# Kernel optimization log

Measured on AMD Instinct MI355X. Metric: run time of the kernel, lower is better.

## Reference

```python
import jax, jax.numpy as jnp
import numpy as np

B, S, D = 4, 2048, 1024
H, HD = 8, 128
EPS = 1e-5
NEG = -1e30


def layernorm(x, w, b):
    mu = jnp.mean(x, axis=-1, keepdims=True)
    var = jnp.mean(jnp.square(x - mu), axis=-1, keepdims=True)
    return (x - mu) * jax.lax.rsqrt(var + EPS) * w + b


def rmsnorm(x, w):
    ms = jnp.mean(jnp.square(x), axis=-1, keepdims=True)
    return x * jax.lax.rsqrt(ms + EPS) * w


def setup_inputs() -> dict:
    key = jax.random.key(0)
    ks = jax.random.split(key, 8)
    scale = 0.02
    return {
        "layer_input": jax.random.normal(ks[0], (B, S, D), jnp.float32),
        "positions": jnp.broadcast_to(jnp.arange(S, dtype=jnp.int32), (B, S)),
        "ln_in_w": jnp.ones((D,), jnp.float32),
        "ln_in_b": jnp.zeros((D,), jnp.float32),
        "W_uvqk": jax.random.normal(ks[1], (D, 4 * H * HD), jnp.float32) * scale,
        "b_uvqk": jax.random.normal(ks[2], (4 * H * HD,), jnp.float32) * scale,
        "ln_out_w": jnp.ones((H * HD,), jnp.float32),
        "ln_out_b": jnp.zeros((H * HD,), jnp.float32),
        "W_proj": jax.random.normal(ks[3], (H * HD, D), jnp.float32) * scale,
        "rms_w": jnp.ones((D,), jnp.float32),
        "W1": jax.random.normal(ks[4], (D, 2 * D), jnp.float32) * scale,
        "W2": jax.random.normal(ks[5], (D, D), jnp.float32) * scale,
    }


def reference(layer_input, positions, ln_in_w, ln_in_b, W_uvqk, b_uvqk,
              ln_out_w, ln_out_b, W_proj, rms_w, W1, W2):
    # --- HSTU attention block ---
    normed = layernorm(layer_input, ln_in_w, ln_in_b)              # [B,S,D]
    mixed = jax.nn.silu(normed @ W_uvqk + b_uvqk)                  # [B,S,4*H*HD]
    user, value, query, key = jnp.split(mixed, 4, axis=-1)
    q = query.reshape(B, S, H, HD)
    k = key.reshape(B, S, H, HD)
    v = value.reshape(B, S, H, HD)
    alpha = 1.0 / np.sqrt(HD).astype(np.float32)
    scores = jnp.einsum("bqhd,bkhd->bhqk", q, k) * alpha           # [B,H,S,S]
    causal = jnp.tril(jnp.ones((S, S), bool))
    scores = jnp.where(causal, scores, NEG)
    probs = jax.nn.softmax(scores, axis=-1)
    attn = jnp.einsum("bhqk,bkhd->bqhd", probs, v).reshape(B, S, H * HD)
    # output norm * user gate, then projection
    parallel = user * layernorm(attn, ln_out_w, ln_out_b)          # [B,S,H*HD]
    layer_output = parallel @ W_proj                               # [B,S,D]
    # --- residual add + RMSNorm + SwiGLU FFN ---
    summed = layer_output + layer_input
    ffn_in = rmsnorm(summed, rms_w)
    h = ffn_in @ W1                                                # [B,S,2D]
    a, b = jnp.split(h, 2, axis=-1)                                # a <- w3, b <- w1
    ffn_out = (jax.nn.silu(a) * b) @ W2
    return ffn_out + layer_output
```

## Files before the change

kernel.cpp:

```cpp
#include <hip/hip_runtime.h>
#include <stdint.h>

typedef unsigned short u16;
typedef __bf16 bf16x8_t __attribute__((ext_vector_type(8)));
typedef float f32x4_t __attribute__((ext_vector_type(4)));

#define D_MODEL 1024
#define SEQ 2048
#define BATCH 4
#define NROWS (BATCH * SEQ)
#define HDIM 128

constexpr int EPI_UVQK = 0;
constexpr int EPI_F32 = 1;
constexpr int EPI_BF16 = 2;
constexpr int EPI_ADD_F32 = 3;

__device__ __forceinline__ float bf2f(u16 u) {
  union { unsigned int i; float f; } v; v.i = ((unsigned int)u) << 16; return v.f;
}
__device__ __forceinline__ u16 f2bf(float f) {
  union { float f; unsigned int i; } v; v.f = f;
  unsigned int r = (v.i + 0x7FFFu + ((v.i >> 16) & 1u)) >> 16;
  return (u16)r;
}
__device__ __forceinline__ float silu_f(float x) { return x / (1.0f + __expf(-x)); }

__device__ __forceinline__ void load_lds16(const void* g, void* l) {
  auto gp = (const __attribute__((address_space(1))) char*)(uintptr_t)g;
  auto lp = (__attribute__((address_space(3))) char*)(uint32_t)(uintptr_t)l;
  __builtin_amdgcn_global_load_lds(gp, lp, 16, 0, 0);
}

__device__ __forceinline__ void block_sum2(float& a, float& b, float* sm) {
  #pragma unroll
  for (int off = 32; off > 0; off >>= 1) {
    a += __shfl_xor(a, off, 64);
    b += __shfl_xor(b, off, 64);
  }
  const int w = threadIdx.x >> 6;
  if ((threadIdx.x & 63) == 0) { sm[w] = a; sm[4 + w] = b; }
  __syncthreads();
  a = sm[0] + sm[1] + sm[2] + sm[3];
  b = sm[4] + sm[5] + sm[6] + sm[7];
}

__global__ __launch_bounds__(256)
void k_wconv(const float* __restrict__ W, u16* __restrict__ Wt, int K, int N) {
  __shared__ float tile[32][33];
  const int n0 = blockIdx.x * 32, k0 = blockIdx.y * 32;
  const int tx = threadIdx.x & 31, ty = threadIdx.x >> 5;
  #pragma unroll
  for (int i = 0; i < 4; i++)
    tile[ty + 8 * i][tx] = W[(size_t)(k0 + ty + 8 * i) * N + n0 + tx];
  __syncthreads();
  #pragma unroll
  for (int i = 0; i < 4; i++)
    Wt[(size_t)(n0 + ty + 8 * i) * K + k0 + tx] = f2bf(tile[tx][ty + 8 * i]);
}

__global__ __launch_bounds__(256)
void k_ln_in(const float* __restrict__ X, const float* __restrict__ w,
             const float* __restrict__ b, u16* __restrict__ Y) {
  __shared__ float sm[8];
  const int row = blockIdx.x, t = threadIdx.x;
  const float4 v = ((const float4*)(X + (size_t)row * D_MODEL))[t];
  float s = v.x + v.y + v.z + v.w;
  float ss = v.x * v.x + v.y * v.y + v.z * v.z + v.w * v.w;
  block_sum2(s, ss, sm);
  const float mu = s * (1.0f / D_MODEL);
  const float var = ss * (1.0f / D_MODEL) - mu * mu;
  const float rs = rsqrtf(var + 1e-5f);
  const float4 wv = ((const float4*)w)[t];
  const float4 bv = ((const float4*)b)[t];
  ushort4 o;
  o.x = f2bf((v.x - mu) * rs * wv.x + bv.x);
  o.y = f2bf((v.y - mu) * rs * wv.y + bv.y);
  o.z = f2bf((v.z - mu) * rs * wv.z + bv.z);
  o.w = f2bf((v.w - mu) * rs * wv.w + bv.w);
  ((ushort4*)(Y + (size_t)row * D_MODEL))[t] = o;
}

__global__ __launch_bounds__(256)
void k_gated(const u16* __restrict__ attn, const u16* __restrict__ mixed,
             const float* __restrict__ w, const float* __restrict__ b,
             u16* __restrict__ out) {
  __shared__ float sm[8];
  const int row = blockIdx.x, t = threadIdx.x;
  const ushort4 av = ((const ushort4*)(attn + (size_t)row * D_MODEL))[t];
  const float x0 = bf2f(av.x), x1 = bf2f(av.y), x2 = bf2f(av.z), x3 = bf2f(av.w);
  float s = x0 + x1 + x2 + x3;
  float ss = x0 * x0 + x1 * x1 + x2 * x2 + x3 * x3;
  block_sum2(s, ss, sm);
  const float mu = s * (1.0f / D_MODEL);
  const float rs = rsqrtf(ss * (1.0f / D_MODEL) - mu * mu + 1e-5f);
  const ushort4 uv = ((const ushort4*)(mixed + (size_t)row * 4096))[t];
  const float4 wv = ((const float4*)w)[t];
  const float4 bv = ((const float4*)b)[t];
  ushort4 o;
  o.x = f2bf(bf2f(uv.x) * ((x0 - mu) * rs * wv.x + bv.x));
  o.y = f2bf(bf2f(uv.y) * ((x1 - mu) * rs * wv.y + bv.y));
  o.z = f2bf(bf2f(uv.z) * ((x2 - mu) * rs * wv.z + bv.z));
  o.w = f2bf(bf2f(uv.w) * ((x3 - mu) * rs * wv.w + bv.w));
  ((ushort4*)(out + (size_t)row * D_MODEL))[t] = o;
}

__global__ __launch_bounds__(256)
void k_rms(const float* __restrict__ lo, const float* __restrict__ li,
           const float* __restrict__ w, u16* __restrict__ out) {
  __shared__ float sm[8];
  const int row = blockIdx.x, t = threadIdx.x;
  const float4 a = ((const float4*)(lo + (size_t)row * D_MODEL))[t];
  const float4 bq = ((const float4*)(li + (size_t)row * D_MODEL))[t];
  const float x0 = a.x + bq.x, x1 = a.y + bq.y, x2 = a.z + bq.z, x3 = a.w + bq.w;
  float ss = x0 * x0 + x1 * x1 + x2 * x2 + x3 * x3, dummy = 0.f;
  block_sum2(ss, dummy, sm);
  const float rs = rsqrtf(ss * (1.0f / D_MODEL) + 1e-5f);
  const float4 wv = ((const float4*)w)[t];
  ushort4 o;
  o.x = f2bf(x0 * rs * wv.x);
  o.y = f2bf(x1 * rs * wv.y);
  o.z = f2bf(x2 * rs * wv.z);
  o.w = f2bf(x3 * rs * wv.w);
  ((ushort4*)(out + (size_t)row * D_MODEL))[t] = o;
}

__global__ __launch_bounds__(256)
void k_silumul(const u16* __restrict__ h, u16* __restrict__ g) {
  const int row = blockIdx.x, t = threadIdx.x;
  const ushort4 a = ((const ushort4*)(h + (size_t)row * 2048))[t];
  const ushort4 b = ((const ushort4*)(h + (size_t)row * 2048 + 1024))[t];
  ushort4 o;
  o.x = f2bf(silu_f(bf2f(a.x)) * bf2f(b.x));
  o.y = f2bf(silu_f(bf2f(a.y)) * bf2f(b.y));
  o.z = f2bf(silu_f(bf2f(a.z)) * bf2f(b.z));
  o.w = f2bf(silu_f(bf2f(a.w)) * bf2f(b.w));
  ((ushort4*)(g + (size_t)row * D_MODEL))[t] = o;
}

template <int EPI>
__global__ __launch_bounds__(256, 2)
void k_gemm(const u16* __restrict__ A, const u16* __restrict__ Bt,
            void* __restrict__ Cout, const float* __restrict__ bias,
            const float* __restrict__ addsrc,
            u16* __restrict__ kc, u16* __restrict__ vtc,
            int M, int N, int K) {
  __shared__ u16 As[128 * 64];
  __shared__ u16 Bs[128 * 64];
  const int t = threadIdx.x, lane = t & 63, w = t >> 6;
  const int l15 = lane & 15, l4 = lane >> 4;
  const int wr = w >> 1, wc = w & 1;
  const int m0 = blockIdx.x * 128, n0 = blockIdx.y * 128;
  const int lr = lane >> 3, lc = lane & 7;
  const int swz = (lc ^ lr) * 8;

  f32x4_t acc[4][4];
  #pragma unroll
  for (int mi = 0; mi < 4; mi++)
    #pragma unroll
    for (int ni = 0; ni < 4; ni++) {
      acc[mi][ni][0] = 0.f; acc[mi][ni][1] = 0.f; acc[mi][ni][2] = 0.f; acc[mi][ni][3] = 0.f;
    }

  const u16* Ab = A + (size_t)m0 * K + swz;
  const u16* Bb = Bt + (size_t)n0 * K + swz;

  for (int kt = 0; kt < K; kt += 64) {
    #pragma unroll
    for (int j = 0; j < 4; j++) {
      const size_t rr = (size_t)((w * 4 + j) * 8 + lr);
      load_lds16(Ab + rr * K + kt, &As[(w * 4 + j) * 512]);
      load_lds16(Bb + rr * K + kt, &Bs[(w * 4 + j) * 512]);
    }
    __syncthreads();
    #pragma unroll
    for (int kk = 0; kk < 2; kk++) {
      bf16x8_t af[4], bf[4];
      #pragma unroll
      for (int mi = 0; mi < 4; mi++) {
        const int row = wr * 64 + mi * 16 + l15;
        const int cph = (kk * 4 + l4) ^ (row & 7);
        af[mi] = *(const bf16x8_t*)&As[row * 64 + cph * 8];
      }
      #pragma unroll
      for (int ni = 0; ni < 4; ni++) {
        const int row = wc * 64 + ni * 16 + l15;
        const int cph = (kk * 4 + l4) ^ (row & 7);
        bf[ni] = *(const bf16x8_t*)&Bs[row * 64 + cph * 8];
      }
      #pragma unroll
      for (int mi = 0; mi < 4; mi++)
        #pragma unroll
        for (int ni = 0; ni < 4; ni++)
          acc[mi][ni] = __builtin_amdgcn_mfma_f32_16x16x32_bf16(af[mi], bf[ni], acc[mi][ni], 0, 0, 0);
    }
    __syncthreads();
  }

  #pragma unroll
  for (int mi = 0; mi < 4; mi++) {
    #pragma unroll
    for (int ni = 0; ni < 4; ni++) {
      const int col = n0 + wc * 64 + ni * 16 + l15;
      float bv = 0.f;
      if constexpr (EPI == EPI_UVQK) bv = bias[col];
      if constexpr (EPI == EPI_UVQK) {
        const int rowb = m0 + wr * 64 + mi * 16 + l4 * 4;
        u16 c4[4];
        #pragma unroll
        for (int r = 0; r < 4; r++) c4[r] = f2bf(silu_f(acc[mi][ni][r] + bv));
        if (col < 1024 || (col >= 2048 && col < 3072)) {
          #pragma unroll
          for (int r = 0; r < 4; r++)
            ((u16*)Cout)[(size_t)(rowb + r) * N + col] = c4[r];
        } else if (col < 2048) {
          const int h = (col - 1024) >> 7, d = (col - 1024) & 127;
          const int bI = rowb >> 11, seqr = rowb & 2047;
          const size_t off = ((size_t)(bI * 8 + h) * 32 + (seqr >> 6)) * 8192 + d * 64 + (seqr & 63);
          *(ushort4*)&vtc[off] = *(const ushort4*)c4;
        } else {
          const int h = (col - 3072) >> 7, d = (col - 3072) & 127;
          const int bI = rowb >> 11, seqr = rowb & 2047;
          #pragma unroll
          for (int r = 0; r < 4; r++)
            kc[((size_t)(bI * 8 + h) * 2048 + seqr + r) * 128 + d] = c4[r];
        }
      } else {
        #pragma unroll
        for (int r = 0; r < 4; r++) {
          const size_t row = (size_t)(m0 + wr * 64 + mi * 16 + l4 * 4 + r);
          float v = acc[mi][ni][r];
          if constexpr (EPI == EPI_BF16) {
            ((u16*)Cout)[row * N + col] = f2bf(v);
          } else if constexpr (EPI == EPI_F32) {
            ((float*)Cout)[row * N + col] = v;
          } else {
            ((float*)Cout)[row * N + col] = v + addsrc[row * N + col];
          }
        }
      }
    }
  }
}

__global__ __launch_bounds__(256, 2)
void k_attn(const u16* __restrict__ mixed, const u16* __restrict__ Kc,
            const u16* __restrict__ Vtc, u16* __restrict__ attnb,
            u16* __restrict__ o_part, float* __restrict__ ml) {
  __shared__ u16 Ks[64 * 128];
  __shared__ u16 Vts[128 * 64];
  __shared__ u16 Ps[4 * 16 * 64];
  const int t = threadIdx.x, lane = t & 63, w = t >> 6;
  const int l15 = lane & 15, l4 = lane >> 4;
  const int f = blockIdx.x;
  const int v = (f & 7) * 96 + (f >> 3);
  const int ci = v % 24, bh = v / 24;
  const int bI = bh >> 3, h = bh & 7;
  int qt, ch;
  if (ci < 16) { qt = 15 - (ci >> 1); ch = ci & 1; }
  else { qt = 23 - ci; ch = 0; }
  const bool split = (qt >= 8);
  const int qb = qt * 128;
  const int nt_all = 2 * qt + 2;
  const int t0 = (split && ch == 1) ? (qt + 1) : 0;
  const int t1 = (split && ch == 0) ? (qt + 1) : nt_all;

  const u16* base = mixed + (size_t)bI * SEQ * 4096;
  const int qcol = 2 * D_MODEL + h * HDIM;
  const int qrow0 = qb + w * 32;
  const u16* Kh = Kc + (size_t)bh * SEQ * 128;
  const u16* Vh = Vtc + (size_t)bh * 32 * 8192;

  const int nk = lane;

  bf16x8_t qf[2][4];
  #pragma unroll
  for (int mi = 0; mi < 2; mi++) {
    const u16* qp = base + (size_t)(qrow0 + mi * 16 + l15) * 4096 + qcol + l4 * 8;
    #pragma unroll
    for (int ks = 0; ks < 4; ks++) qf[mi][ks] = *(const bf16x8_t*)(qp + ks * 32);
  }

  f32x4_t o[2][8];
  #pragma unroll
  for (int mi = 0; mi < 2; mi++)
    #pragma unroll
    for (int df = 0; df < 8; df++) { o[mi][df][0] = 0.f; o[mi][df][1] = 0.f; o[mi][df][2] = 0.f; o[mi][df][3] = 0.f; }
  float mrun[2][4], lrun[2][4];
  #pragma unroll
  for (int mi = 0; mi < 2; mi++)
    #pragma unroll
    for (int r = 0; r < 4; r++) { mrun[mi][r] = -1e30f; lrun[mi][r] = 0.f; }

  const float alpha = 0.08838834764831845f;

  auto stage = [&](int tile) {
    const u16* Kt = Kh + (size_t)(tile * 64) * 128;
    const u16* Vt = Vh + (size_t)tile * 8192;
    #pragma unroll
    for (int j = 0; j < 4; j++) {
      const int slot = j * 4 + w;
      const int kr = slot * 4 + (nk >> 4), gk = nk & 15;
      load_lds16(Kt + kr * 128 + ((gk ^ (kr & 7)) * 8), &Ks[slot * 512]);
      const int d = slot * 8 + (nk >> 3), gv = nk & 7;
      load_lds16(Vt + d * 64 + ((gv ^ (d & 7) ^ ((d >> 3) & 7)) * 8), &Vts[slot * 512]);
    }
  };

  for (int it = t0; it < t1; it++) {
    const int kb = it * 64;
    stage(it);
    __syncthreads();

    const bool active = (kb <= qrow0 + 31);
    const bool needmask = (kb + 63 > qrow0);
    if (active) {
      f32x4_t s[2][4];
      #pragma unroll
      for (int mi = 0; mi < 2; mi++)
        #pragma unroll
        for (int ni = 0; ni < 4; ni++) { s[mi][ni][0] = 0.f; s[mi][ni][1] = 0.f; s[mi][ni][2] = 0.f; s[mi][ni][3] = 0.f; }
      #pragma unroll
      for (int ks = 0; ks < 4; ks++) {
        bf16x8_t kf[4];
        #pragma unroll
        for (int ni = 0; ni < 4; ni++) {
          const int key = ni * 16 + l15;
          const int cph = (ks * 4 + l4) ^ (key & 7);
          kf[ni] = *(const bf16x8_t*)&Ks[key * 128 + cph * 8];
        }
        #pragma unroll
        for (int mi = 0; mi < 2; mi++)
          #pragma unroll
          for (int ni = 0; ni < 4; ni++)
            s[mi][ni] = __builtin_amdgcn_mfma_f32_16x16x32_bf16(qf[mi][ks], kf[ni], s[mi][ni], 0, 0, 0);
      }
      #pragma unroll
      for (int mi = 0; mi < 2; mi++) {
        #pragma unroll
        for (int r = 0; r < 4; r++) {
          const int qr = qrow0 + mi * 16 + l4 * 4 + r;
          float mx = -1e30f;
          #pragma unroll
          for (int ni = 0; ni < 4; ni++) {
            float v2 = s[mi][ni][r] * alpha;
            if (needmask) {
              const int key = kb + ni * 16 + l15;
              if (key > qr) v2 = -1e30f;
            }
            s[mi][ni][r] = v2;
            mx = fmaxf(mx, v2);
          }
          #pragma unroll
          for (int off = 1; off < 16; off <<= 1) mx = fmaxf(mx, __shfl_xor(mx, off, 64));
          const float mnew = fmaxf(mrun[mi][r], mx);
          const float fsc = __expf(mrun[mi][r] - mnew);
          mrun[mi][r] = mnew;
          lrun[mi][r] *= fsc;
          #pragma unroll
          for (int df = 0; df < 8; df++) o[mi][df][r] *= fsc;
          float ls = 0.f;
          #pragma unroll
          for (int ni = 0; ni < 4; ni++) {
            const float p = __expf(s[mi][ni][r] - mnew);
            s[mi][ni][r] = p;
            ls += p;
          }
          #pragma unroll
          for (int off = 1; off < 16; off <<= 1) ls += __shfl_xor(ls, off, 64);
          lrun[mi][r] += ls;
        }
        #pragma unroll
        for (int ni = 0; ni < 4; ni++)
          #pragma unroll
          for (int r = 0; r < 4; r++) {
            const int pr = l4 * 4 + r;
            const int pc = ni * 16 + l15;
            Ps[w * 1024 + pr * 64 + (((pc >> 3) ^ (pr & 7)) * 8) + (pc & 7)] = f2bf(s[mi][ni][r]);
          }
        #pragma unroll
        for (int ks2 = 0; ks2 < 2; ks2++) {
          bf16x8_t pa;
          {
            const int pr = l15;
            const int cph = (ks2 * 4 + l4) ^ (pr & 7);
            pa = *(const bf16x8_t*)&Ps[w * 1024 + pr * 64 + cph * 8];
          }
          #pragma unroll
          for (int df = 0; df < 8; df++) {
            const int d = df * 16 + l15;
            const int cph = (ks2 * 4 + l4) ^ (d & 7) ^ ((d >> 3) & 7);
            const bf16x8_t vb = *(const bf16x8_t*)&Vts[d * 64 + cph * 8];
            o[mi][df] = __builtin_amdgcn_mfma_f32_16x16x32_bf16(pa, vb, o[mi][df], 0, 0, 0);
          }
        }
      }
    }
    __syncthreads();
  }

  if (!split) {
    #pragma unroll
    for (int mi = 0; mi < 2; mi++) {
      #pragma unroll
      for (int r = 0; r < 4; r++) {
        const float inv = 1.0f / lrun[mi][r];
        const size_t row = (size_t)bI * SEQ + qrow0 + mi * 16 + l4 * 4 + r;
        #pragma unroll
        for (int df = 0; df < 8; df++)
          attnb[row * D_MODEL + h * HDIM + df * 16 + l15] = f2bf(o[mi][df][r] * inv);
      }
    }
  } else {
    const int sl = bh * 8 + (qt - 8);
    #pragma unroll
    for (int mi = 0; mi < 2; mi++) {
      #pragma unroll
      for (int r = 0; r < 4; r++) {
        const int pr = w * 32 + mi * 16 + l4 * 4 + r;
        if (l15 == 0) {
          ml[sl * 512 + ch * 256 + pr] = mrun[mi][r];
          ml[sl * 512 + ch * 256 + 128 + pr] = lrun[mi][r];
        }
        if (ch == 0) {
          const size_t row = (size_t)bI * SEQ + qb + pr;
          #pragma unroll
          for (int df = 0; df < 8; df++)
            attnb[row * D_MODEL + h * HDIM + df * 16 + l15] = f2bf(o[mi][df][r]);
        } else {
          #pragma unroll
          for (int df = 0; df < 8; df++)
            o_part[(size_t)sl * 16384 + pr * 128 + df * 16 + l15] = f2bf(o[mi][df][r]);
        }
      }
    }
  }
}

__global__ __launch_bounds__(256)
void k_combine(const u16* __restrict__ o_part, const float* __restrict__ ml,
               u16* __restrict__ attnb) {
  const int qti = blockIdx.x, bh = blockIdx.y;
  const int bI = bh >> 3, h = bh & 7;
  const int t = threadIdx.x;
  const int pr = t >> 1, half = t & 1;
  const int sl = bh * 8 + qti;
  const float m0 = ml[sl * 512 + pr];
  const float l0 = ml[sl * 512 + 128 + pr];
  const float m1 = ml[sl * 512 + 256 + pr];
  const float l1 = ml[sl * 512 + 384 + pr];
  const float M = fmaxf(m0, m1);
  const float w0 = __expf(m0 - M), w1 = __expf(m1 - M);
  const float inv = 1.0f / (w0 * l0 + w1 * l1);
  const float c0 = w0 * inv, c1 = w1 * inv;
  const size_t row = (size_t)bI * SEQ + (8 + qti) * 128 + pr;
  u16* ap = attnb + row * D_MODEL + h * HDIM + half * 64;
  const u16* pp = o_part + (size_t)sl * 16384 + pr * 128 + half * 64;
  #pragma unroll
  for (int j = 0; j < 8; j++) {
    u16 a[8], b[8], c[8];
    *(uint4*)a = ((const uint4*)ap)[j];
    *(uint4*)b = ((const uint4*)pp)[j];
    #pragma unroll
    for (int i = 0; i < 8; i++) c[i] = f2bf(c0 * bf2f(a[i]) + c1 * bf2f(b[i]));
    ((uint4*)ap)[j] = *(const uint4*)c;
  }
}

extern "C" void kernel_launch(void* const* d_in, const int* in_sizes, int n_in,
                              void* d_out, int out_size, void* d_ws, size_t ws_size,
                              hipStream_t stream) {
  (void)in_sizes; (void)n_in; (void)out_size; (void)ws_size;
  const float* layer_input = (const float*)d_in[0];
  const float* ln_in_w  = (const float*)d_in[2];
  const float* ln_in_b  = (const float*)d_in[3];
  const float* W_uvqk   = (const float*)d_in[4];
  const float* b_uvqk   = (const float*)d_in[5];
  const float* ln_out_w = (const float*)d_in[6];
  const float* ln_out_b = (const float*)d_in[7];
  const float* W_proj   = (const float*)d_in[8];
  const float* rms_w    = (const float*)d_in[9];
  const float* W1       = (const float*)d_in[10];
  const float* W2       = (const float*)d_in[11];
  float* out = (float*)d_out;

  char* ws = (char*)d_ws;
  u16* buf0    = (u16*)(ws);
  u16* mixed   = (u16*)(ws + ((size_t)16 << 20));
  u16* attnb   = (u16*)(ws + ((size_t)80 << 20));
  float* lout  = (float*)(ws + ((size_t)96 << 20));
  u16* Kc      = (u16*)(ws + ((size_t)96 << 20));
  u16* Vtc     = (u16*)(ws + ((size_t)112 << 20));
  u16* wt_uvqk = (u16*)(ws + ((size_t)128 << 20));
  u16* wt_proj = (u16*)(ws + ((size_t)136 << 20));
  u16* wt_1    = (u16*)(ws + ((size_t)138 << 20));
  u16* wt_2    = (u16*)(ws + ((size_t)142 << 20));
  u16* o_part  = (u16*)d_out;
  float* ml    = (float*)((char*)d_out + ((size_t)20 << 20));

  k_wconv<<<dim3(128, 32), 256, 0, stream>>>(W_uvqk, wt_uvqk, 1024, 4096);
  k_wconv<<<dim3(32, 32), 256, 0, stream>>>(W_proj, wt_proj, 1024, 1024);
  k_wconv<<<dim3(64, 32), 256, 0, stream>>>(W1, wt_1, 1024, 2048);
  k_wconv<<<dim3(32, 32), 256, 0, stream>>>(W2, wt_2, 1024, 1024);

  k_ln_in<<<NROWS, 256, 0, stream>>>(layer_input, ln_in_w, ln_in_b, buf0);
  k_gemm<EPI_UVQK><<<dim3(64, 32), 256, 0, stream>>>(buf0, wt_uvqk, mixed, b_uvqk, nullptr, Kc, Vtc, NROWS, 4096, 1024);
  k_attn<<<768, 256, 0, stream>>>(mixed, Kc, Vtc, attnb, o_part, ml);
  k_combine<<<dim3(8, 32), 256, 0, stream>>>(o_part, ml, attnb);
  k_gated<<<NROWS, 256, 0, stream>>>(attnb, mixed, ln_out_w, ln_out_b, buf0);
  k_gemm<EPI_F32><<<dim3(64, 8), 256, 0, stream>>>(buf0, wt_proj, lout, nullptr, nullptr, nullptr, nullptr, NROWS, 1024, 1024);
  k_rms<<<NROWS, 256, 0, stream>>>(lout, layer_input, rms_w, buf0);
  k_gemm<EPI_BF16><<<dim3(64, 16), 256, 0, stream>>>(buf0, wt_1, mixed, nullptr, nullptr, nullptr, nullptr, NROWS, 2048, 1024);
  k_silumul<<<NROWS, 256, 0, stream>>>(mixed, buf0);
  k_gemm<EPI_ADD_F32><<<dim3(64, 8), 256, 0, stream>>>(buf0, wt_2, out, nullptr, lout, nullptr, nullptr, NROWS, 1024, 1024);
}
```

Measured before the change: 370.4 us.

## Fuse SwiGLU into W1 GEMM epilogue via interleaved weight rows

The W1 weight is permuted during bf16 conversion so that each 32-row group holds 16 gate rows followed by 16 up rows. Each GEMM tile therefore holds matching gate and up columns, and the epilogue can compute silu(a)*b directly and write the 1024-wide bf16 result. This drops the separate silumul kernel and the write and re-read of the 2048-wide intermediate. The cost is a more complex weight-prep mapping and a dependency on the tile layout of the GEMM.

```diff
diff --git a/kernel.cpp b/kernel.cpp
--- a/kernel.cpp
+++ b/kernel.cpp
@@ -13,7 +13,7 @@
 
 constexpr int EPI_UVQK = 0;
 constexpr int EPI_F32 = 1;
-constexpr int EPI_BF16 = 2;
+constexpr int EPI_SILUMUL = 2;
 constexpr int EPI_ADD_F32 = 3;
 
 __device__ __forceinline__ float bf2f(u16 u) {
@@ -45,6 +45,7 @@
   b = sm[4] + sm[5] + sm[6] + sm[7];
 }
 
+template <int ILV>
 __global__ __launch_bounds__(256)
 void k_wconv(const float* __restrict__ W, u16* __restrict__ Wt, int K, int N) {
   __shared__ float tile[32][33];
@@ -55,8 +56,14 @@
     tile[ty + 8 * i][tx] = W[(size_t)(k0 + ty + 8 * i) * N + n0 + tx];
   __syncthreads();
   #pragma unroll
-  for (int i = 0; i < 4; i++)
-    Wt[(size_t)(n0 + ty + 8 * i) * K + k0 + tx] = f2bf(tile[tx][ty + 8 * i]);
+  for (int i = 0; i < 4; i++) {
+    const int nlog = n0 + ty + 8 * i;
+    int rowp;
+    if (ILV == 0) rowp = nlog;
+    else rowp = (nlog < 1024) ? (32 * (nlog >> 4) + (nlog & 15))
+                              : (32 * ((nlog - 1024) >> 4) + 16 + ((nlog - 1024) & 15));
+    Wt[(size_t)rowp * K + k0 + tx] = f2bf(tile[tx][ty + 8 * i]);
+  }
 }
 
 __global__ __launch_bounds__(256)
@@ -125,19 +132,6 @@
   ((ushort4*)(out + (size_t)row * D_MODEL))[t] = o;
 }
 
-__global__ __launch_bounds__(256)
-void k_silumul(const u16* __restrict__ h, u16* __restrict__ g) {
-  const int row = blockIdx.x, t = threadIdx.x;
-  const ushort4 a = ((const ushort4*)(h + (size_t)row * 2048))[t];
-  const ushort4 b = ((const ushort4*)(h + (size_t)row * 2048 + 1024))[t];
-  ushort4 o;
-  o.x = f2bf(silu_f(bf2f(a.x)) * bf2f(b.x));
-  o.y = f2bf(silu_f(bf2f(a.y)) * bf2f(b.y));
-  o.z = f2bf(silu_f(bf2f(a.z)) * bf2f(b.z));
-  o.w = f2bf(silu_f(bf2f(a.w)) * bf2f(b.w));
-  ((ushort4*)(g + (size_t)row * D_MODEL))[t] = o;
-}
-
 template <int EPI>
 __global__ __launch_bounds__(256, 2)
 void k_gemm(const u16* __restrict__ A, const u16* __restrict__ Bt,
@@ -197,45 +191,58 @@
     __syncthreads();
   }
 
-  #pragma unroll
-  for (int mi = 0; mi < 4; mi++) {
-    #pragma unroll
-    for (int ni = 0; ni < 4; ni++) {
-      const int col = n0 + wc * 64 + ni * 16 + l15;
-      float bv = 0.f;
-      if constexpr (EPI == EPI_UVQK) bv = bias[col];
-      if constexpr (EPI == EPI_UVQK) {
-        const int rowb = m0 + wr * 64 + mi * 16 + l4 * 4;
-        u16 c4[4];
-        #pragma unroll
-        for (int r = 0; r < 4; r++) c4[r] = f2bf(silu_f(acc[mi][ni][r] + bv));
-        if (col < 1024 || (col >= 2048 && col < 3072)) {
-          #pragma unroll
-          for (int r = 0; r < 4; r++)
-            ((u16*)Cout)[(size_t)(rowb + r) * N + col] = c4[r];
-        } else if (col < 2048) {
-          const int h = (col - 1024) >> 7, d = (col - 1024) & 127;
-          const int bI = rowb >> 11, seqr = rowb & 2047;
-          const size_t off = ((size_t)(bI * 8 + h) * 32 + (seqr >> 6)) * 8192 + d * 64 + (seqr & 63);
-          *(ushort4*)&vtc[off] = *(const ushort4*)c4;
-        } else {
-          const int h = (col - 3072) >> 7, d = (col - 3072) & 127;
-          const int bI = rowb >> 11, seqr = rowb & 2047;
-          #pragma unroll
-          for (int r = 0; r < 4; r++)
-            kc[((size_t)(bI * 8 + h) * 2048 + seqr + r) * 128 + d] = c4[r];
-        }
-      } else {
+  if constexpr (EPI == EPI_SILUMUL) {
+    #pragma unroll
+    for (int mi = 0; mi < 4; mi++)
+      #pragma unroll
+      for (int nj = 0; nj < 2; nj++) {
+        const int gcol = (n0 >> 1) + wc * 32 + nj * 16 + l15;
         #pragma unroll
         for (int r = 0; r < 4; r++) {
           const size_t row = (size_t)(m0 + wr * 64 + mi * 16 + l4 * 4 + r);
-          float v = acc[mi][ni][r];
-          if constexpr (EPI == EPI_BF16) {
-            ((u16*)Cout)[row * N + col] = f2bf(v);
-          } else if constexpr (EPI == EPI_F32) {
-            ((float*)Cout)[row * N + col] = v;
+          ((u16*)Cout)[row * 1024 + gcol] =
+              f2bf(silu_f(acc[mi][2 * nj][r]) * acc[mi][2 * nj + 1][r]);
+        }
+      }
+  } else {
+    #pragma unroll
+    for (int mi = 0; mi < 4; mi++) {
+      #pragma unroll
+      for (int ni = 0; ni < 4; ni++) {
+        const int col = n0 + wc * 64 + ni * 16 + l15;
+        float bv = 0.f;
+        if constexpr (EPI == EPI_UVQK) bv = bias[col];
+        if constexpr (EPI == EPI_UVQK) {
+          const int rowb = m0 + wr * 64 + mi * 16 + l4 * 4;
+          u16 c4[4];
+          #pragma unroll
+          for (int r = 0; r < 4; r++) c4[r] = f2bf(silu_f(acc[mi][ni][r] + bv));
+          if (col < 1024 || (col >= 2048 && col < 3072)) {
+            #pragma unroll
+            for (int r = 0; r < 4; r++)
+              ((u16*)Cout)[(size_t)(rowb + r) * N + col] = c4[r];
+          } else if (col < 2048) {
+            const int h = (col - 1024) >> 7, d = (col - 1024) & 127;
+            const int bI = rowb >> 11, seqr = rowb & 2047;
+            const size_t off = ((size_t)(bI * 8 + h) * 32 + (seqr >> 6)) * 8192 + d * 64 + (seqr & 63);
+            *(ushort4*)&vtc[off] = *(const ushort4*)c4;
           } else {
-            ((float*)Cout)[row * N + col] = v + addsrc[row * N + col];
+            const int h = (col - 3072) >> 7, d = (col - 3072) & 127;
+            const int bI = rowb >> 11, seqr = rowb & 2047;
+            #pragma unroll
+            for (int r = 0; r < 4; r++)
+              kc[((size_t)(bI * 8 + h) * 2048 + seqr + r) * 128 + d] = c4[r];
+          }
+        } else {
+          #pragma unroll
+          for (int r = 0; r < 4; r++) {
+            const size_t row = (size_t)(m0 + wr * 64 + mi * 16 + l4 * 4 + r);
+            float v = acc[mi][ni][r];
+            if constexpr (EPI == EPI_F32) {
+              ((float*)Cout)[row * N + col] = v;
+            } else {
+              ((float*)Cout)[row * N + col] = v + addsrc[row * N + col];
+            }
           }
         }
       }
@@ -498,10 +505,10 @@
   u16* o_part  = (u16*)d_out;
   float* ml    = (float*)((char*)d_out + ((size_t)20 << 20));
 
-  k_wconv<<<dim3(128, 32), 256, 0, stream>>>(W_uvqk, wt_uvqk, 1024, 4096);
-  k_wconv<<<dim3(32, 32), 256, 0, stream>>>(W_proj, wt_proj, 1024, 1024);
-  k_wconv<<<dim3(64, 32), 256, 0, stream>>>(W1, wt_1, 1024, 2048);
-  k_wconv<<<dim3(32, 32), 256, 0, stream>>>(W2, wt_2, 1024, 1024);
+  k_wconv<0><<<dim3(128, 32), 256, 0, stream>>>(W_uvqk, wt_uvqk, 1024, 4096);
+  k_wconv<0><<<dim3(32, 32), 256, 0, stream>>>(W_proj, wt_proj, 1024, 1024);
+  k_wconv<1><<<dim3(64, 32), 256, 0, stream>>>(W1, wt_1, 1024, 2048);
+  k_wconv<0><<<dim3(32, 32), 256, 0, stream>>>(W2, wt_2, 1024, 1024);
 
   k_ln_in<<<NROWS, 256, 0, stream>>>(layer_input, ln_in_w, ln_in_b, buf0);
   k_gemm<EPI_UVQK><<<dim3(64, 32), 256, 0, stream>>>(buf0, wt_uvqk, mixed, b_uvqk, nullptr, Kc, Vtc, NROWS, 4096, 1024);
@@ -510,7 +517,6 @@
   k_gated<<<NROWS, 256, 0, stream>>>(attnb, mixed, ln_out_w, ln_out_b, buf0);
   k_gemm<EPI_F32><<<dim3(64, 8), 256, 0, stream>>>(buf0, wt_proj, lout, nullptr, nullptr, nullptr, nullptr, NROWS, 1024, 1024);
   k_rms<<<NROWS, 256, 0, stream>>>(lout, layer_input, rms_w, buf0);
-  k_gemm<EPI_BF16><<<dim3(64, 16), 256, 0, stream>>>(buf0, wt_1, mixed, nullptr, nullptr, nullptr, nullptr, NROWS, 2048, 1024);
-  k_silumul<<<NROWS, 256, 0, stream>>>(mixed, buf0);
-  k_gemm<EPI_ADD_F32><<<dim3(64, 8), 256, 0, stream>>>(buf0, wt_2, out, nullptr, lout, nullptr, nullptr, NROWS, 1024, 1024);
-}
+  k_gemm<EPI_SILUMUL><<<dim3(64, 16), 256, 0, stream>>>(buf0, wt_1, mixed, nullptr, nullptr, nullptr, nullptr, NROWS, 2048, 1024);
+  k_gemm<EPI_ADD_F32><<<dim3(64, 8), 256, 0, stream>>>(mixed, wt_2, out, nullptr, lout, nullptr, nullptr, NROWS, 1024, 1024);
+}
```

Measured after the change: 360.6 us. -2.7%, faster.
